# Kernel optimization log

Measured on AMD Instinct MI355X. Metric: run time of the kernel, lower is better.

Reference implementation:

```python
import jax, jax.numpy as jnp
import numpy as np

B, T, C = 2, 2048, 2048
H = 16
D = C // H  # 128 head dim
EPS = 1.1920929e-07  # torch RMSNorm default eps for fp32 (finfo.eps)
ROPE_BASE = 1000000.0


def setup_inputs() -> dict:
    key = jax.random.key(0)
    k1, k2, k3 = jax.random.split(key, 3)
    x = jax.random.normal(k1, (B, T, C), dtype=jnp.float32)
    w_qkv = jax.random.normal(k2, (C, 3 * C), dtype=jnp.float32) * (C ** -0.5)
    w_proj = jax.random.normal(k3, (C, C), dtype=jnp.float32) * (C ** -0.5)
    q_norm_w = jnp.ones((D,), dtype=jnp.float32)
    k_norm_w = jnp.ones((D,), dtype=jnp.float32)
    return {"x": x, "w_qkv": w_qkv, "w_proj": w_proj,
            "q_norm_w": q_norm_w, "k_norm_w": k_norm_w}


def _rms_norm(x, w):
    var = jnp.mean(jnp.square(x), axis=-1, keepdims=True)
    return x * jax.lax.rsqrt(var + EPS) * w


def _rope_tables(t_len, d_head, dtype):
    inv_freq = 1.0 / (ROPE_BASE ** (jnp.arange(0, d_head, 2, dtype=jnp.float32) / d_head))
    t = jnp.arange(t_len, dtype=jnp.float32)
    freqs = jnp.einsum('i,j->ij', t, inv_freq)          # [T, D/2]
    emb = jnp.concatenate([freqs, freqs], axis=-1)      # [T, D]
    return jnp.cos(emb).astype(dtype), jnp.sin(emb).astype(dtype)


def _rotate_half(x):
    x1, x2 = x[..., : x.shape[-1] // 2], x[..., x.shape[-1] // 2:]
    return jnp.concatenate([-x2, x1], axis=-1)


def reference(x, w_qkv, w_proj, q_norm_w, k_norm_w):
    b, t, c = x.shape
    qkv = x @ w_qkv                                     # [B, T, 3C]
    q, k, v = jnp.split(qkv, 3, axis=-1)
    # [B, H, T, D]
    q = q.reshape(b, t, H, D).transpose(0, 2, 1, 3)
    k = k.reshape(b, t, H, D).transpose(0, 2, 1, 3)
    v = v.reshape(b, t, H, D).transpose(0, 2, 1, 3)
    q = _rms_norm(q, q_norm_w)
    k = _rms_norm(k, k_norm_w)
    cos, sin = _rope_tables(t, D, x.dtype)              # [T, D]
    q = q * cos + _rotate_half(q) * sin
    k = k * cos + _rotate_half(k) * sin
    # NOTE: module uses scale = 1/d_head, not 1/sqrt(d_head)
    scale = 1.0 / D
    att = jnp.einsum('bhqd,bhkd->bhqk', q, k) * scale   # [B, H, T, T]
    causal = jnp.tril(jnp.ones((t, t), dtype=bool))
    att = jnp.where(causal, att, jnp.finfo(att.dtype).min)
    att = jax.nn.softmax(att, axis=-1)
    y = jnp.einsum('bhqk,bhkd->bhqd', att, v)           # [B, H, T, D]
    y = y.transpose(0, 2, 1, 3).reshape(b, t, c)
    return y @ w_proj
```

## Files before the change

### kernel.cpp

```cpp
#include <hip/hip_runtime.h>
#include <stdint.h>

#define Bb   2
#define Tt   2048
#define Cc_  2048
#define Hh   16
#define Dd   128
#define Mm_  4096
#define N1   6144
#define EPSf 1.1920929e-07f
#define SCALE (1.0f/128.0f)

typedef __bf16 bf16;
typedef __attribute__((ext_vector_type(8))) __bf16 bf16x8;
typedef __attribute__((ext_vector_type(4))) float  f32x4;

__device__ __forceinline__ void gl_lds16(const bf16* g, bf16* l) {
  __builtin_amdgcn_global_load_lds(
      (const __attribute__((address_space(1))) unsigned int*)g,
      (__attribute__((address_space(3))) unsigned int*)l, 16, 0, 0);
}

__global__ __launch_bounds__(256) void cvt_bf16(const float* __restrict__ in,
                                                bf16* __restrict__ out, int n) {
  int i = (blockIdx.x * 256 + threadIdx.x) * 4;
  if (i >= n) return;
  float4 v = *(const float4*)(in + i);
  union { bf16 h[4]; uint2 u; } o;
  o.h[0] = (bf16)v.x; o.h[1] = (bf16)v.y; o.h[2] = (bf16)v.z; o.h[3] = (bf16)v.w;
  *(uint2*)(out + i) = o.u;
}

__global__ __launch_bounds__(256) void transpose_cvt(const float* __restrict__ in,
                                                     bf16* __restrict__ out,
                                                     int R, int Cc) {
  __shared__ float tile[64][65];
  int c0 = blockIdx.x * 64, r0 = blockIdx.y * 64;
  int tid = threadIdx.x;
#pragma unroll
  for (int j = 0; j < 16; ++j) {
    int idx = tid + j * 256;
    int r = idx >> 6, c = idx & 63;
    tile[r][c] = in[(size_t)(r0 + r) * Cc + c0 + c];
  }
  __syncthreads();
#pragma unroll
  for (int j = 0; j < 16; ++j) {
    int idx = tid + j * 256;
    int rr = idx & 63, cc = idx >> 6;
    out[(size_t)(c0 + cc) * R + r0 + rr] = (bf16)tile[rr][cc];
  }
}

__global__ __launch_bounds__(256) void vtrans(const bf16* __restrict__ V,
                                              bf16* __restrict__ Vt_) {
  __shared__ bf16 tile[64][72];
  int bh = blockIdx.z, t0 = blockIdx.x * 64, d0 = blockIdx.y * 64;
  int tid = threadIdx.x;
#pragma unroll
  for (int j = 0; j < 2; ++j) {
    int idx = (j * 256 + tid) * 8;
    int r = idx >> 6, c = idx & 63;
    bf16x8 v = *(const bf16x8*)(V + ((size_t)bh * Tt + t0 + r) * Dd + d0 + c);
#pragma unroll
    for (int e = 0; e < 8; ++e) tile[r][c + e] = v[e];
  }
  __syncthreads();
#pragma unroll
  for (int j = 0; j < 2; ++j) {
    int idx = (j * 256 + tid) * 8;
    int dd = idx >> 6, tt = idx & 63;
    bf16x8 v;
#pragma unroll
    for (int e = 0; e < 8; ++e) v[e] = tile[tt + e][dd];
    *(bf16x8*)(Vt_ + ((size_t)bh * Dd + d0 + dd) * Tt + t0 + tt) = v;
  }
}

template <typename OutT>
__global__ __launch_bounds__(256) void gemm_bf16(const bf16* __restrict__ A,
                                                 const bf16* __restrict__ Bt,
                                                 OutT* __restrict__ Cm,
                                                 int Nn, int Kk) {
  __shared__ __align__(16) bf16 As[128 * 64];
  __shared__ __align__(16) bf16 Bs[128 * 64];
  const int tid = threadIdx.x;
  const int wave = tid >> 6, lane = tid & 63;
  const int quad = lane >> 4, li = lane & 15;
  const int wm = wave >> 1, wn = wave & 1;
  const int m0 = blockIdx.y * 128, n0 = blockIdx.x * 128;

  f32x4 acc[4][4] = {};

  for (int kt = 0; kt < Kk; kt += 64) {
    __syncthreads();
#pragma unroll
    for (int j = 0; j < 4; ++j) {
      int c = j * 256 + tid;
      int r = c >> 3, cc = c & 7;
      int gc = ((cc ^ (r & 7)) << 3);
      gl_lds16(A + (size_t)(m0 + r) * Kk + kt + gc, &As[c * 8]);
      gl_lds16(Bt + (size_t)(n0 + r) * Kk + kt + gc, &Bs[c * 8]);
    }
    __syncthreads();
#pragma unroll
    for (int kc = 0; kc < 2; ++kc) {
      bf16x8 af[4], bfr[4];
#pragma unroll
      for (int t = 0; t < 4; ++t) {
        int rowa = wm * 64 + t * 16 + li;
        af[t] = *(const bf16x8*)&As[rowa * 64 + (((kc * 4 + quad) ^ (rowa & 7)) << 3)];
        int rowb = wn * 64 + t * 16 + li;
        bfr[t] = *(const bf16x8*)&Bs[rowb * 64 + (((kc * 4 + quad) ^ (rowb & 7)) << 3)];
      }
#pragma unroll
      for (int mi = 0; mi < 4; ++mi)
#pragma unroll
        for (int ni = 0; ni < 4; ++ni)
          acc[mi][ni] = __builtin_amdgcn_mfma_f32_16x16x32_bf16(af[mi], bfr[ni],
                                                                acc[mi][ni], 0, 0, 0);
    }
  }
#pragma unroll
  for (int mi = 0; mi < 4; ++mi) {
    int row = m0 + wm * 64 + mi * 16 + quad * 4;
#pragma unroll
    for (int ni = 0; ni < 4; ++ni) {
      int col = n0 + wn * 64 + ni * 16 + li;
#pragma unroll
      for (int r = 0; r < 4; ++r)
        Cm[(size_t)(row + r) * Nn + col] = (OutT)acc[mi][ni][r];
    }
  }
}

__global__ __launch_bounds__(512, 2) void gemm256(const bf16* __restrict__ A,
                                                  const bf16* __restrict__ Bt,
                                                  bf16* __restrict__ Cm,
                                                  int Nn, int Kk) {
  __shared__ __align__(16) bf16 As[2][256 * 64];
  __shared__ __align__(16) bf16 Bs[2][256 * 64];
  const int tid = threadIdx.x;
  const int wave = tid >> 6, lane = tid & 63;
  const int quad = lane >> 4, li = lane & 15;
  const int wm = wave >> 2, wn = wave & 3;

  const int nwg = gridDim.x * gridDim.y;
  const int wg  = blockIdx.y * gridDim.x + blockIdx.x;
  const int swz = (wg & 7) * (nwg >> 3) + (wg >> 3);
  const int m0 = (swz / gridDim.x) * 256;
  const int n0 = (swz % gridDim.x) * 256;

  const int NT = Kk >> 6;
  const int lrow = lane >> 3;
  const int lchk = (lane & 7) ^ lrow;

  auto stageA = [&](int tt, int h, int cb) {
    int kt = (tt < NT ? tt : NT - 1) << 6;
#pragma unroll
    for (int j = 0; j < 2; ++j) {
      int seg = j * 8 + wave;
      int r0 = ((seg >> 3) << 7) + (h << 6) + ((seg & 7) << 3);
      gl_lds16(A + (size_t)(m0 + r0 + lrow) * Kk + kt + (lchk << 3),
               &As[cb][r0 * 64]);
    }
  };
  auto stageB = [&](int tt, int h, int cb) {
    int kt = (tt < NT ? tt : NT - 1) << 6;
#pragma unroll
    for (int j = 0; j < 2; ++j) {
      int seg = j * 8 + wave;
      int r0 = ((seg >> 2) << 6) + (h << 5) + ((seg & 3) << 3);
      gl_lds16(Bt + (size_t)(n0 + r0 + lrow) * Kk + kt + (lchk << 3),
               &Bs[cb][r0 * 64]);
    }
  };

  f32x4 acc[8][4] = {};
  bf16x8 afr[4][2], bfr[2][2];

  auto rdA = [&](int h, int cb) {
#pragma unroll
    for (int mi = 0; mi < 4; ++mi) {
      int r = wm * 128 + h * 64 + mi * 16 + li;
#pragma unroll
      for (int kc = 0; kc < 2; ++kc)
        afr[mi][kc] = *(const bf16x8*)&As[cb][r * 64 + (((kc * 4 + quad) ^ (r & 7)) << 3)];
    }
  };
  auto rdB = [&](int h, int cb) {
#pragma unroll
    for (int nj = 0; nj < 2; ++nj) {
      int r = wn * 64 + h * 32 + nj * 16 + li;
#pragma unroll
      for (int kc = 0; kc < 2; ++kc)
        bfr[nj][kc] = *(const bf16x8*)&Bs[cb][r * 64 + (((kc * 4 + quad) ^ (r & 7)) << 3)];
    }
  };
  auto mmac = [&](int mo, int no) {
    __builtin_amdgcn_s_setprio(1);
#pragma unroll
    for (int kc = 0; kc < 2; ++kc)
#pragma unroll
      for (int mi = 0; mi < 4; ++mi)
#pragma unroll
        for (int nj = 0; nj < 2; ++nj)
          acc[mo + mi][no + nj] = __builtin_amdgcn_mfma_f32_16x16x32_bf16(
              afr[mi][kc], bfr[nj][kc], acc[mo + mi][no + nj], 0, 0, 0);
    __builtin_amdgcn_s_setprio(0);
  };

  stageA(0, 0, 0); stageB(0, 0, 0); stageB(0, 1, 0); stageA(0, 1, 0);
  stageA(1, 0, 1); stageB(1, 1, 1);
  asm volatile("s_waitcnt vmcnt(4)" ::: "memory");
  __builtin_amdgcn_s_barrier();

  for (int t = 0; t < NT; ++t) {
    const int cur = t & 1, nxt = cur ^ 1;
    rdA(0, cur); rdB(0, cur);
    stageB(t + 1, 0, nxt);
    __builtin_amdgcn_s_barrier();
    asm volatile("s_waitcnt lgkmcnt(0)" ::: "memory");
    __builtin_amdgcn_sched_barrier(0);
    mmac(0, 0);
    __builtin_amdgcn_s_barrier();
    rdB(1, cur);
    stageA(t + 1, 1, nxt);
    __builtin_amdgcn_s_barrier();
    asm volatile("s_waitcnt lgkmcnt(0)" ::: "memory");
    __builtin_amdgcn_sched_barrier(0);
    mmac(0, 2);
    __builtin_amdgcn_s_barrier();
    rdA(1, cur);
    stageA(t + 2, 0, cur);
    __builtin_amdgcn_s_barrier();
    asm volatile("s_waitcnt lgkmcnt(0)" ::: "memory");
    __builtin_amdgcn_sched_barrier(0);
    mmac(4, 2);
    __builtin_amdgcn_s_barrier();
    rdB(0, cur);
    stageB(t + 2, 1, cur);
    __builtin_amdgcn_s_barrier();
    asm volatile("s_waitcnt lgkmcnt(0)" ::: "memory");
    __builtin_amdgcn_sched_barrier(0);
    mmac(4, 0);
    asm volatile("s_waitcnt vmcnt(4)" ::: "memory");
    __builtin_amdgcn_s_barrier();
  }
  asm volatile("s_waitcnt vmcnt(0)" ::: "memory");

#pragma unroll
  for (int mi = 0; mi < 8; ++mi) {
    int row = m0 + wm * 128 + mi * 16 + quad * 4;
#pragma unroll
    for (int nj = 0; nj < 4; ++nj) {
      int col = n0 + wn * 64 + nj * 16 + li;
#pragma unroll
      for (int r = 0; r < 4; ++r)
        Cm[(size_t)(row + r) * Nn + col] = (bf16)acc[mi][nj][r];
    }
  }
}

__global__ __launch_bounds__(256) void norm_rope_rearrange(
    const bf16* __restrict__ qkv, const float* __restrict__ qw,
    const float* __restrict__ kw, bf16* __restrict__ Qg,
    bf16* __restrict__ Kg, bf16* __restrict__ Vg) {
  int unit = blockIdx.x * 4 + (threadIdx.x >> 6);
  int lane = threadIdx.x & 63;
  int h = unit & 15;
  int bt = unit >> 4;
  int t = bt & 2047, b = bt >> 11;
  const bf16* base = qkv + (size_t)bt * N1 + h * Dd;
  float q1 = (float)base[lane], q2 = (float)base[lane + 64];
  float k1 = (float)base[Cc_ + lane], k2 = (float)base[Cc_ + lane + 64];
  float v1 = (float)base[2 * Cc_ + lane], v2 = (float)base[2 * Cc_ + lane + 64];
  float sq = q1 * q1 + q2 * q2;
  float sk = k1 * k1 + k2 * k2;
#pragma unroll
  for (int o = 1; o < 64; o <<= 1) { sq += __shfl_xor(sq, o); sk += __shfl_xor(sk, o); }
  float rq = rsqrtf(sq * (1.0f / 128.0f) + EPSf);
  float rk = rsqrtf(sk * (1.0f / 128.0f) + EPSf);
  q1 *= rq * qw[lane]; q2 *= rq * qw[lane + 64];
  k1 *= rk * kw[lane]; k2 *= rk * kw[lane + 64];
  float invf = exp2f((float)lane * (-19.9315685693241740f / 64.0f));
  float ang = (float)t * invf;
  float sn, cs;
  sincosf(ang, &sn, &cs);
  float qo1 = q1 * cs - q2 * sn, qo2 = q2 * cs + q1 * sn;
  float ko1 = k1 * cs - k2 * sn, ko2 = k2 * cs + k1 * sn;
  size_t o1 = ((size_t)(b * Hh + h) * Tt + t) * Dd + lane;
  Qg[o1] = (bf16)qo1; Qg[o1 + 64] = (bf16)qo2;
  Kg[o1] = (bf16)ko1; Kg[o1 + 64] = (bf16)ko2;
  Vg[o1] = (bf16)v1;  Vg[o1 + 64] = (bf16)v2;
}

__global__ __launch_bounds__(256, 3) void attn(const bf16* __restrict__ Qg,
                                               const bf16* __restrict__ Kg,
                                               const bf16* __restrict__ VgT,
                                               bf16* __restrict__ Yg) {
  __shared__ __align__(16) bf16 Kl[64 * 128];
  __shared__ __align__(16) bf16 Vl[128 * 64];
  __shared__ __align__(16) bf16 Pl[4 * 16 * 72];
  const int bh = blockIdx.x;
  const int qt = (int)gridDim.y - 1 - (int)blockIdx.y;
  const int b = bh >> 4, h = bh & 15;
  const int tid = threadIdx.x, wave = tid >> 6, lane = tid & 63;
  const int quad = lane >> 4, li = lane & 15;
  const int q0 = qt * 64;

  const bf16* Qbase = Qg + ((size_t)bh * Tt + q0 + wave * 16 + li) * Dd;
  bf16x8 qf[4];
#pragma unroll
  for (int kc = 0; kc < 4; ++kc) qf[kc] = *(const bf16x8*)(Qbase + kc * 32 + quad * 8);

  f32x4 o[8] = {};
  float L[4] = {};
  bf16* Pw = &Pl[wave * 16 * 72];

  for (int kt = 0; kt <= qt; ++kt) {
    const int k0 = kt * 64;
    __syncthreads();
#pragma unroll
    for (int j = 0; j < 4; ++j) {
      int c = j * 256 + tid;
      int r = c >> 4, cc = c & 15;
      gl_lds16(Kg + ((size_t)bh * Tt + k0 + r) * Dd + ((cc ^ (r & 7)) << 3), &Kl[c * 8]);
    }
#pragma unroll
    for (int j = 0; j < 4; ++j) {
      int c = j * 256 + tid;
      int r = c >> 3, cc = c & 7;
      gl_lds16(VgT + ((size_t)bh * Dd + r) * Tt + k0 + ((cc ^ (r & 7)) << 3), &Vl[c * 8]);
    }
    __syncthreads();

    f32x4 s4[4] = {};
#pragma unroll
    for (int nt = 0; nt < 4; ++nt) {
      int key = nt * 16 + li;
#pragma unroll
      for (int kc = 0; kc < 4; ++kc) {
        bf16x8 kf = *(const bf16x8*)&Kl[key * 128 + (((kc * 4 + quad) ^ (key & 7)) << 3)];
        s4[nt] = __builtin_amdgcn_mfma_f32_16x16x32_bf16(qf[kc], kf, s4[nt], 0, 0, 0);
      }
    }
    const bool diag = (kt == qt);
#pragma unroll
    for (int nt = 0; nt < 4; ++nt)
#pragma unroll
      for (int r = 0; r < 4; ++r) {
        float e = __expf(s4[nt][r] * SCALE);
        if (diag && (nt * 16 + li > wave * 16 + quad * 4 + r)) e = 0.f;
        L[r] += e;
        Pw[(quad * 4 + r) * 72 + nt * 16 + li] = (bf16)e;
      }
#pragma unroll
    for (int kc = 0; kc < 2; ++kc) {
      bf16x8 pf = *(const bf16x8*)&Pw[li * 72 + kc * 32 + quad * 8];
#pragma unroll
      for (int u = 0; u < 8; ++u) {
        bf16x8 vf = *(const bf16x8*)&Vl[(u * 16 + li) * 64 + (((kc * 4 + quad) ^ (li & 7)) << 3)];
        o[u] = __builtin_amdgcn_mfma_f32_16x16x32_bf16(pf, vf, o[u], 0, 0, 0);
      }
    }
  }

  float inv[4];
#pragma unroll
  for (int r = 0; r < 4; ++r) {
    float s0 = L[r];
#pragma unroll
    for (int off = 1; off < 16; off <<= 1) s0 += __shfl_xor(s0, off);
    inv[r] = 1.0f / s0;
  }
  int trow = q0 + wave * 16 + quad * 4;
#pragma unroll
  for (int u = 0; u < 8; ++u) {
    int col = h * Dd + u * 16 + li;
#pragma unroll
    for (int r = 0; r < 4; ++r)
      Yg[(size_t)(b * Tt + trow + r) * Cc_ + col] = (bf16)(o[u][r] * inv[r]);
  }
}

extern "C" void kernel_launch(void* const* d_in, const int* in_sizes, int n_in,
                              void* d_out, int out_size, void* d_ws, size_t ws_size,
                              hipStream_t stream) {
  const float* x      = (const float*)d_in[0];
  const float* w_qkv  = (const float*)d_in[1];
  const float* w_proj = (const float*)d_in[2];
  const float* qnw    = (const float*)d_in[3];
  const float* knw    = (const float*)d_in[4];
  float* out = (float*)d_out;

  bf16* xb     = (bf16*)d_ws;
  bf16* wqkvT  = xb + (size_t)Mm_ * Cc_;
  bf16* wprojT = wqkvT + (size_t)N1 * Cc_;
  bf16* qkv    = wprojT + (size_t)Cc_ * Cc_;
  bf16* Qg     = qkv + (size_t)Mm_ * N1;
  bf16* Kg     = Qg + (size_t)Bb * Hh * Tt * Dd;
  bf16* Vg     = Kg + (size_t)Bb * Hh * Tt * Dd;
  bf16* VgT    = xb;
  bf16* Yg     = qkv;

  hipLaunchKernelGGL(cvt_bf16, dim3((Mm_ * Cc_ / 4) / 256), dim3(256), 0, stream,
                     x, xb, Mm_ * Cc_);
  hipLaunchKernelGGL(transpose_cvt, dim3(N1 / 64, Cc_ / 64), dim3(256), 0, stream,
                     w_qkv, wqkvT, Cc_, N1);
  hipLaunchKernelGGL(transpose_cvt, dim3(Cc_ / 64, Cc_ / 64), dim3(256), 0, stream,
                     w_proj, wprojT, Cc_, Cc_);
  hipLaunchKernelGGL(gemm256, dim3(N1 / 256, Mm_ / 256), dim3(512), 0, stream,
                     xb, wqkvT, qkv, N1, Cc_);
  hipLaunchKernelGGL(norm_rope_rearrange, dim3(Bb * Tt * Hh / 4), dim3(256), 0, stream,
                     qkv, qnw, knw, Qg, Kg, Vg);
  hipLaunchKernelGGL(vtrans, dim3(Tt / 64, Dd / 64, Bb * Hh), dim3(256), 0, stream,
                     Vg, VgT);
  hipLaunchKernelGGL(attn, dim3(Bb * Hh, Tt / 64), dim3(256), 0, stream,
                     Qg, Kg, VgT, Yg);
  hipLaunchKernelGGL(gemm_bf16<float>, dim3(Cc_ / 128, Mm_ / 128), dim3(256), 0, stream,
                     Yg, wprojT, out, Cc_, Cc_);
}
```

Measured before the change: 410.8 us.

## Keep both B fragment halves in registers and reschedule GEMM LDS staging

Splits the B fragment registers into two sets so the first B half is kept and reused for the last MFMA quadrant instead of being re-read from LDS. The global-to-LDS staging order is rearranged so more loads are in flight (vmcnt raised to 6), and the loop is unrolled by two with fixed buffer indices. This aims to cut LDS reads and barrier stalls in the GEMM main loop. It costs more VGPRs and assumes NT is even.

```diff
diff --git a/kernel.cpp b/kernel.cpp
--- a/kernel.cpp
+++ b/kernel.cpp
@@ -177,7 +177,7 @@
   };
 
   f32x4 acc[8][4] = {};
-  bf16x8 afr[4][2], bfr[2][2];
+  bf16x8 afr[4][2], b0r[2][2], b1r[2][2];
 
   auto rdA = [&](int h, int cb) {
 #pragma unroll
@@ -188,16 +188,16 @@
         afr[mi][kc] = *(const bf16x8*)&As[cb][r * 64 + (((kc * 4 + quad) ^ (r & 7)) << 3)];
     }
   };
-  auto rdB = [&](int h, int cb) {
+  auto rdB = [&](int h, int cb, bf16x8 (&dst)[2][2]) {
 #pragma unroll
     for (int nj = 0; nj < 2; ++nj) {
       int r = wn * 64 + h * 32 + nj * 16 + li;
 #pragma unroll
       for (int kc = 0; kc < 2; ++kc)
-        bfr[nj][kc] = *(const bf16x8*)&Bs[cb][r * 64 + (((kc * 4 + quad) ^ (r & 7)) << 3)];
-    }
-  };
-  auto mmac = [&](int mo, int no) {
+        dst[nj][kc] = *(const bf16x8*)&Bs[cb][r * 64 + (((kc * 4 + quad) ^ (r & 7)) << 3)];
+    }
+  };
+  auto mmac = [&](int mo, int no, bf16x8 (&b)[2][2]) {
     __builtin_amdgcn_s_setprio(1);
 #pragma unroll
     for (int kc = 0; kc < 2; ++kc)
@@ -206,46 +206,49 @@
 #pragma unroll
         for (int nj = 0; nj < 2; ++nj)
           acc[mo + mi][no + nj] = __builtin_amdgcn_mfma_f32_16x16x32_bf16(
-              afr[mi][kc], bfr[nj][kc], acc[mo + mi][no + nj], 0, 0, 0);
+              afr[mi][kc], b[nj][kc], acc[mo + mi][no + nj], 0, 0, 0);
     __builtin_amdgcn_s_setprio(0);
   };
 
-  stageA(0, 0, 0); stageB(0, 0, 0); stageB(0, 1, 0); stageA(0, 1, 0);
-  stageA(1, 0, 1); stageB(1, 1, 1);
-  asm volatile("s_waitcnt vmcnt(4)" ::: "memory");
-  __builtin_amdgcn_s_barrier();
-
-  for (int t = 0; t < NT; ++t) {
-    const int cur = t & 1, nxt = cur ^ 1;
-    rdA(0, cur); rdB(0, cur);
-    stageB(t + 1, 0, nxt);
+  auto tile = [&](int t, int cur, int nxt) {
+    rdA(0, cur); rdB(0, cur, b0r);
+    stageA(t + 1, 1, nxt);
+    asm volatile("s_waitcnt lgkmcnt(8)" ::: "memory");
     __builtin_amdgcn_s_barrier();
     asm volatile("s_waitcnt lgkmcnt(0)" ::: "memory");
     __builtin_amdgcn_sched_barrier(0);
-    mmac(0, 0);
-    __builtin_amdgcn_s_barrier();
-    rdB(1, cur);
-    stageA(t + 1, 1, nxt);
+    mmac(0, 0, b0r);
+    __builtin_amdgcn_s_barrier();
+    rdB(1, cur, b1r);
+    stageA(t + 2, 0, cur);
     __builtin_amdgcn_s_barrier();
     asm volatile("s_waitcnt lgkmcnt(0)" ::: "memory");
     __builtin_amdgcn_sched_barrier(0);
-    mmac(0, 2);
+    mmac(0, 2, b1r);
     __builtin_amdgcn_s_barrier();
     rdA(1, cur);
-    stageA(t + 2, 0, cur);
+    stageB(t + 2, 0, cur);
     __builtin_amdgcn_s_barrier();
     asm volatile("s_waitcnt lgkmcnt(0)" ::: "memory");
     __builtin_amdgcn_sched_barrier(0);
-    mmac(4, 2);
-    __builtin_amdgcn_s_barrier();
-    rdB(0, cur);
+    mmac(4, 2, b1r);
+    __builtin_amdgcn_s_barrier();
     stageB(t + 2, 1, cur);
     __builtin_amdgcn_s_barrier();
-    asm volatile("s_waitcnt lgkmcnt(0)" ::: "memory");
     __builtin_amdgcn_sched_barrier(0);
-    mmac(4, 0);
-    asm volatile("s_waitcnt vmcnt(4)" ::: "memory");
-    __builtin_amdgcn_s_barrier();
+    mmac(4, 0, b0r);
+    asm volatile("s_waitcnt vmcnt(6)" ::: "memory");
+    __builtin_amdgcn_s_barrier();
+  };
+
+  stageA(0, 0, 0); stageB(0, 0, 0); stageB(0, 1, 0); stageA(0, 1, 0);
+  stageA(1, 0, 1); stageB(1, 0, 1); stageB(1, 1, 1);
+  asm volatile("s_waitcnt vmcnt(6)" ::: "memory");
+  __builtin_amdgcn_s_barrier();
+
+  for (int t = 0; t < NT; t += 2) {
+    tile(t, 0, 1);
+    tile(t + 1, 1, 0);
   }
   asm volatile("s_waitcnt vmcnt(0)" ::: "memory");
 
```

Result: faster. 391.0 us (-4.8%).
